# Kernel optimization log

Hardware: AMD Instinct MI355X
Metric: run time of the kernel (lower is better)

## Reference

```python
import jax, jax.numpy as jnp
import numpy as np

V, D, F, K, L, R, ID, B = 50000, 64, 100, 3, 256, 10, 32, 128
IDMAX = 50


def _cnn(vec, Wc, bc, Wl, bl):
    # vec: [N, L, D] -> Conv1d over L (channels=D), ReLU, max-pool over L, Linear+tanh
    x = vec.transpose(0, 2, 1)  # [N, D, L]
    pad = (K - 1) // 2
    y = jax.lax.conv_general_dilated(x, Wc, (1,), [(pad, pad)],
                                     dimension_numbers=('NCH', 'OIH', 'NCH'))
    y = jax.nn.relu(y + bc[None, :, None])  # [N, F, L]
    y = y.max(axis=2)  # [N, F]
    return jnp.tanh(y @ Wl.T + bl)  # [N, ID]


def _fm(x, v, w, b):
    lin = x @ w.T + b  # [N, 1]
    i1 = x @ v
    i2 = (x ** 2) @ (v ** 2)
    pair = jnp.sum(i1 ** 2 - i2, axis=1)
    return (lin[:, 0] + 0.5 * pair)[:, None]


def setup_inputs() -> dict:
    key = jax.random.key(0)
    ks = iter(jax.random.split(key, 40))
    nrm = lambda shape, s=0.1: jax.random.normal(next(ks), shape, jnp.float32) * s
    ri = lambda shape, hi: jax.random.randint(next(ks), shape, 0, hi, dtype=jnp.int32)
    return dict(
        user_reviews=ri((B, R, L), V), item_reviews=ri((B, R, L), V),
        uids=ri((B,), IDMAX), iids=ri((B,), IDMAX),
        user2item=ri((B, R), IDMAX), item2user=ri((B, R), IDMAX),
        rand_reviews=ri((B, L), V),
        user_emb=nrm((V, D)), item_emb=nrm((V, D)),
        cu_Wc=nrm((F, D, K)), cu_bc=jnp.zeros((F,)), cu_Wl=nrm((ID, F)), cu_bl=jnp.zeros((ID,)),
        ci_Wc=nrm((F, D, K)), ci_bc=jnp.zeros((F,)), ci_Wl=nrm((ID, F)), ci_bl=jnp.zeros((ID,)),
        t_W1=nrm((ID, 2 * R * ID)), t_b1=jnp.full((ID,), 0.1),
        t_W2=nrm((ID, ID)), t_b2=jnp.full((ID,), 0.1),
        fs_v=jnp.full((ID, 8), 0.001), fs_w=nrm((1, ID), 0.001), fs_b=jnp.zeros((1,)),
        te_emb=nrm((V, D)),
        tc_Wc=nrm((F, D, K)), tc_bc=jnp.zeros((F,)), tc_Wl=nrm((ID, F)), tc_bl=jnp.zeros((ID,)),
        ft_v=jnp.full((ID, 8), 0.001), ft_w=nrm((1, ID), 0.001), ft_b=jnp.zeros((1,)),
    )


def reference(user_reviews, item_reviews, uids, iids, user2item, item2user, rand_reviews,
              user_emb, item_emb, cu_Wc, cu_bc, cu_Wl, cu_bl, ci_Wc, ci_bc, ci_Wl, ci_bl,
              t_W1, t_b1, t_W2, t_b2, fs_v, fs_w, fs_b,
              te_emb, tc_Wc, tc_bc, tc_Wl, tc_bl, ft_v, ft_w, ft_b):
    Bn = user_reviews.shape[0]
    ur = user_reviews.reshape(Bn * R, L)
    ir = item_reviews.reshape(Bn * R, L)
    # SourceNet
    ul = _cnn(user_emb[ur], cu_Wc, cu_bc, cu_Wl, cu_bl).reshape(Bn, R * ID)
    il = _cnn(item_emb[ir], ci_Wc, ci_bc, ci_Wl, ci_bl).reshape(Bn, R * ID)
    cat = jnp.concatenate([ul, il], axis=1)  # [B, 2*R*ID]
    h = jnp.tanh(cat @ t_W1.T + t_b1)
    src = jnp.tanh(h @ t_W2.T + t_b2)  # dropout in eval mode = identity
    _src_pred = _fm(jax.lax.stop_gradient(src), fs_v, fs_w, fs_b)  # computed, unused in output
    # Vectorized replacement of the per-sample membership/gather loop
    mu = user2item == iids[:, None]  # [B, R]
    mi = item2user == uids[:, None]  # [B, R]
    gu = user_reviews[jnp.arange(Bn), jnp.argmax(mu, axis=1)]  # first match
    gi = item_reviews[jnp.arange(Bn), jnp.argmax(mi, axis=1)]
    reviews = jnp.where(mu.any(1)[:, None], gu,
                        jnp.where(mi.any(1)[:, None], gi, rand_reviews))  # [B, L]
    # TargetNet
    tl = _cnn(te_emb[reviews], tc_Wc, tc_bc, tc_Wl, tc_bl)
    _tgt_pred = _fm(tl, ft_v, ft_w, ft_b)  # computed, unused in output
    return src, tl
```

## Files before the change

kernel.cpp:

```cpp
#include <hip/hip_runtime.h>
#include <hip/hip_bf16.h>


#define C_V 50000
#define C_D 64
#define C_F 100
#define C_K 3
#define C_L 256
#define C_R 10
#define C_ID 32
#define C_B 128

typedef unsigned int u32;
typedef unsigned short u16;
typedef __attribute__((ext_vector_type(8))) short bf16x8;
typedef __attribute__((ext_vector_type(4))) float f32x4;

__device__ __forceinline__ float bf2f(u16 h) { union {u32 u; float f;} v; v.u = ((u32)h) << 16; return v.f; }
__device__ __forceinline__ u16 f2bf(float f) {
    union {float f; u32 u;} v; v.f = f;
    u32 u = v.u;
    return (u16)((u + 0x7fffu + ((u >> 16) & 1u)) >> 16);
}
__device__ __forceinline__ float ldf(const void* p, int idx, int isf) {
    return isf ? ((const float*)p)[idx] : bf2f(((const u16*)p)[idx]);
}
__device__ __forceinline__ void stf(void* p, int idx, float v, int isf) {
    if (isf) ((float*)p)[idx] = v; else ((u16*)p)[idx] = f2bf(v);
}
__device__ __forceinline__ int detect_isf(const u32* __restrict__ ue, int lane) {
    u32 w = ue[lane];
    u32 e = (w >> 7) & 0xFFu;
    int hit = (e >= 0x70u && e <= 0x7Fu);
    unsigned long long m = __ballot(hit);
    return (__popcll(m) >= 32) ? 0 : 1;
}
__device__ __forceinline__ void gl_lds16(const void* g, void* l) {
    __builtin_amdgcn_global_load_lds(
        (const __attribute__((address_space(1))) void*)g,
        (__attribute__((address_space(3))) void*)l, 16, 0, 0);
}

__global__ __launch_bounds__(256) void prep_bfrags(
    const void* __restrict__ cu_Wc, const void* __restrict__ ci_Wc,
    const void* __restrict__ tc_Wc, const u32* __restrict__ ue,
    u16* __restrict__ wsB)
{
    int tid = threadIdx.x;
    int isf = detect_isf(ue, tid & 63);
    int id = blockIdx.x * 256 + tid;
    if (id >= 3 * 6 * 7 * 64) return;
    int s    = id / 2688;
    int rem  = id % 2688;
    int c    = rem / 448;
    int rem2 = rem % 448;
    int nt   = rem2 / 64;
    int lane = rem2 % 64;
    int f    = nt * 16 + (lane & 15);
    int quad = lane >> 4;
    const void* W = (s == 0) ? cu_Wc : (s == 1) ? ci_Wc : tc_Wc;
    u16 out[8];
    #pragma unroll
    for (int j = 0; j < 8; ++j) {
        int kdim = c * 32 + quad * 8 + j;
        int tap = kdim >> 6, d = kdim & 63;
        float v = (f < C_F) ? ldf(W, (f * C_D + d) * C_K + tap, isf) : 0.f;
        out[j] = f2bf(v);
    }
    *reinterpret_cast<uint4*>(wsB + id * 8) = *reinterpret_cast<const uint4*>(out);
}

__global__ __launch_bounds__(256, 4) void cnn_mfma(
    const int* __restrict__ user_reviews, const int* __restrict__ item_reviews,
    const int* __restrict__ uids, const int* __restrict__ iids,
    const int* __restrict__ user2item, const int* __restrict__ item2user,
    const int* __restrict__ rand_reviews,
    const void* __restrict__ user_emb, const void* __restrict__ item_emb,
    const void* __restrict__ te_emb,
    const void* __restrict__ cu_bc, const void* __restrict__ cu_Wl, const void* __restrict__ cu_bl,
    const void* __restrict__ ci_bc, const void* __restrict__ ci_Wl, const void* __restrict__ ci_bl,
    const void* __restrict__ tc_bc, const void* __restrict__ tc_Wl, const void* __restrict__ tc_bl,
    const u16* __restrict__ wsB,
    float* __restrict__ ws_cat, void* __restrict__ d_out)
{
    __shared__ __align__(16) char smem[258 * 128 + 1600];
    u16*   embS  = (u16*)smem;
    float* poolS = (float*)(smem + 258 * 128);
    float* partS = (float*)smem;

    const int tid = threadIdx.x;
    const int idx = (blockIdx.x & 7) * 336 + (blockIdx.x >> 3);
    const int lane = tid & 63, wave = tid >> 6;
    const int isf = detect_isf((const u32*)user_emb, lane);

    const int* toks;
    const void* emb;
    int set;
    const void *bc, *Wl, *bl;

    if (idx < C_B * C_R) {
        toks = user_reviews + idx * C_L;
        emb = user_emb; set = 0;
        bc = cu_bc; Wl = cu_Wl; bl = cu_bl;
    } else if (idx < 2 * C_B * C_R) {
        int j = idx - C_B * C_R;
        toks = item_reviews + j * C_L;
        emb = item_emb; set = 1;
        bc = ci_bc; Wl = ci_Wl; bl = ci_bl;
    } else {
        int b = idx - 2 * C_B * C_R;
        const int* t_ = rand_reviews + b * C_L;
        int iid = iids[b];
        int uid = uids[b];
        int fu = -1, fi = -1;
        for (int r = C_R - 1; r >= 0; --r) {
            if (user2item[b * C_R + r] == iid) fu = r;
            if (item2user[b * C_R + r] == uid) fi = r;
        }
        if (fu >= 0)      t_ = user_reviews + (b * C_R + fu) * C_L;
        else if (fi >= 0) t_ = item_reviews + (b * C_R + fi) * C_L;
        toks = t_;
        emb = te_emb; set = 2;
        bc = tc_bc; Wl = tc_Wl; bl = tc_bl;
    }

    if (tid < 32)            ((u32*)embS)[tid] = 0u;
    else if (tid < 64)       ((u32*)embS)[257 * 32 + (tid - 32)] = 0u;

    if (!isf) {
        int tok64 = toks[wave * 64 + lane];
        const u16* ebp = (const u16*)emb;
        #pragma unroll
        for (int i = 0; i < 8; ++i) {
            int sub = lane >> 3;
            int token = __shfl(tok64, i * 8 + sub);
            int row_lds = wave * 64 + i * 8 + sub + 1;
            int schunk = (lane & 7) ^ (row_lds & 7);
            const void* g = ebp + (size_t)token * C_D + schunk * 8;
            u16* ldsbase = embS + (size_t)(wave * 64 + i * 8 + 1) * 64;
            gl_lds16(g, ldsbase);
        }
    } else {
        int token = toks[tid];
        int rw = (tid + 1) & 7;
        u16* dst = embS + (size_t)(tid + 1) * 64;
        const float4* srow = reinterpret_cast<const float4*>(
            (const float*)emb + (size_t)token * C_D);
        #pragma unroll
        for (int c = 0; c < 8; ++c) {
            float4 a = srow[2 * c];
            float4 b = srow[2 * c + 1];
            u16 t[8] = {f2bf(a.x), f2bf(a.y), f2bf(a.z), f2bf(a.w),
                        f2bf(b.x), f2bf(b.y), f2bf(b.z), f2bf(b.w)};
            *reinterpret_cast<uint4*>(dst + (c ^ rw) * 8) =
                *reinterpret_cast<const uint4*>(t);
        }
    }
    __syncthreads();

    const int quad = lane >> 4, mcol = lane & 15;
    const int mbase = wave * 64;
    const u16* BfG = wsB + set * 21504;

    {
        f32x4 acc[4][4];
        #pragma unroll
        for (int mt = 0; mt < 4; ++mt)
            #pragma unroll
            for (int nt = 0; nt < 4; ++nt) acc[mt][nt] = (f32x4){0.f,0.f,0.f,0.f};
        #pragma unroll
        for (int c = 0; c < 6; ++c) {
            const int tap = c >> 1, dh = c & 1;
            const int schunk = (dh * 4 + quad) ^ ((mcol + tap) & 7);
            bf16x8 bfr[4];
            #pragma unroll
            for (int nt = 0; nt < 4; ++nt)
                bfr[nt] = *reinterpret_cast<const bf16x8*>(BfG + ((c * 7 + nt) * 64 + lane) * 8);
            bf16x8 afr[4];
            #pragma unroll
            for (int mt = 0; mt < 4; ++mt) {
                int row = mbase + mt * 16 + mcol + tap;
                afr[mt] = *reinterpret_cast<const bf16x8*>(embS + row * 64 + schunk * 8);
            }
            #pragma unroll
            for (int mt = 0; mt < 4; ++mt)
                #pragma unroll
                for (int nt = 0; nt < 4; ++nt)
                    acc[mt][nt] = __builtin_amdgcn_mfma_f32_16x16x32_bf16(
                        afr[mt], bfr[nt], acc[mt][nt], 0, 0, 0);
        }
        #pragma unroll
        for (int nt = 0; nt < 4; ++nt) {
            float mv = -1e30f;
            #pragma unroll
            for (int mt = 0; mt < 4; ++mt)
                mv = fmaxf(mv, fmaxf(fmaxf(acc[mt][nt].x, acc[mt][nt].y),
                                     fmaxf(acc[mt][nt].z, acc[mt][nt].w)));
            mv = fmaxf(mv, __shfl_xor(mv, 16));
            mv = fmaxf(mv, __shfl_xor(mv, 32));
            if (quad == 0) poolS[(nt * 16 + mcol) * 4 + wave] = mv;
        }
    }
    {
        f32x4 acc[4][3];
        #pragma unroll
        for (int mt = 0; mt < 4; ++mt)
            #pragma unroll
            for (int nt = 0; nt < 3; ++nt) acc[mt][nt] = (f32x4){0.f,0.f,0.f,0.f};
        #pragma unroll
        for (int c = 0; c < 6; ++c) {
            const int tap = c >> 1, dh = c & 1;
            const int schunk = (dh * 4 + quad) ^ ((mcol + tap) & 7);
            bf16x8 bfr[3];
            #pragma unroll
            for (int nt = 0; nt < 3; ++nt)
                bfr[nt] = *reinterpret_cast<const bf16x8*>(BfG + ((c * 7 + 4 + nt) * 64 + lane) * 8);
            bf16x8 afr[4];
            #pragma unroll
            for (int mt = 0; mt < 4; ++mt) {
                int row = mbase + mt * 16 + mcol + tap;
                afr[mt] = *reinterpret_cast<const bf16x8*>(embS + row * 64 + schunk * 8);
            }
            #pragma unroll
            for (int mt = 0; mt < 4; ++mt)
                #pragma unroll
                for (int nt = 0; nt < 3; ++nt)
                    acc[mt][nt] = __builtin_amdgcn_mfma_f32_16x16x32_bf16(
                        afr[mt], bfr[nt], acc[mt][nt], 0, 0, 0);
        }
        #pragma unroll
        for (int nt = 0; nt < 3; ++nt) {
            float mv = -1e30f;
            #pragma unroll
            for (int mt = 0; mt < 4; ++mt)
                mv = fmaxf(mv, fmaxf(fmaxf(acc[mt][nt].x, acc[mt][nt].y),
                                     fmaxf(acc[mt][nt].z, acc[mt][nt].w)));
            mv = fmaxf(mv, __shfl_xor(mv, 16));
            mv = fmaxf(mv, __shfl_xor(mv, 32));
            int f = (4 + nt) * 16 + mcol;
            if (quad == 0 && f < C_F) poolS[f * 4 + wave] = mv;
        }
    }
    __syncthreads();

    if (tid < C_F) {
        float m4 = fmaxf(fmaxf(poolS[tid * 4 + 0], poolS[tid * 4 + 1]),
                         fmaxf(poolS[tid * 4 + 2], poolS[tid * 4 + 3]));
        poolS[tid * 4] = fmaxf(m4 + ldf(bc, tid, isf), 0.f);
    }
    __syncthreads();

    {
        int o = tid >> 3, seg = tid & 7;
        int f0 = (seg < 4) ? seg * 13 : 52 + (seg - 4) * 12;
        int cnt = (seg < 4) ? 13 : 12;
        float acc = 0.f;
        for (int q = 0; q < cnt; ++q) {
            int f = f0 + q;
            acc += poolS[f * 4] * ldf(Wl, o * C_F + f, isf);
        }
        partS[o * 8 + seg] = acc;
    }
    __syncthreads();
    if (tid < C_ID) {
        float s = ldf(bl, tid, isf);
        #pragma unroll
        for (int q = 0; q < 8; ++q) s += partS[tid * 8 + q];
        float v = tanhf(s);
        if (idx < C_B * C_R) {
            int b = idx / C_R, r = idx % C_R;
            ws_cat[b * 640 + r * C_ID + tid] = v;
        } else if (idx < 2 * C_B * C_R) {
            int j = idx - C_B * C_R;
            int b = j / C_R, r = j % C_R;
            ws_cat[b * 640 + 320 + r * C_ID + tid] = v;
        } else {
            int b = idx - 2 * C_B * C_R;
            stf(d_out, C_B * C_ID + b * C_ID + tid, v, isf);
        }
    }
}

__global__ __launch_bounds__(256) void head_kernel(
    const float* __restrict__ ws_cat,
    const void* __restrict__ W1, const void* __restrict__ b1,
    const void* __restrict__ W2, const void* __restrict__ b2,
    const u32* __restrict__ ue, void* __restrict__ d_out)
{
    __shared__ float part[C_ID][8];
    __shared__ float h_s[C_ID];
    int b = blockIdx.x;
    int tid = threadIdx.x;
    int isf = detect_isf(ue, tid & 63);
    int o = tid >> 3, seg = tid & 7;
    const float* cat = ws_cat + b * 640;
    float acc = 0.f;
    int j0 = seg * 80;
    for (int j = j0; j < j0 + 80; ++j) acc += cat[j] * ldf(W1, o * 640 + j, isf);
    part[o][seg] = acc;
    __syncthreads();
    if (tid < C_ID) {
        float s = ldf(b1, tid, isf);
        #pragma unroll
        for (int q = 0; q < 8; ++q) s += part[tid][q];
        h_s[tid] = tanhf(s);
    }
    __syncthreads();
    if (tid < C_ID) {
        float s = ldf(b2, tid, isf);
        #pragma unroll
        for (int i = 0; i < C_ID; ++i) s += h_s[i] * ldf(W2, tid * C_ID + i, isf);
        stf(d_out, b * C_ID + tid, tanhf(s), isf);
    }
}

extern "C" void kernel_launch(void* const* d_in, const int* in_sizes, int n_in,
                              void* d_out, int out_size, void* d_ws, size_t ws_size,
                              hipStream_t stream)
{
    const int* user_reviews = (const int*)d_in[0];
    const int* item_reviews = (const int*)d_in[1];
    const int* uids         = (const int*)d_in[2];
    const int* iids         = (const int*)d_in[3];
    const int* user2item    = (const int*)d_in[4];
    const int* item2user    = (const int*)d_in[5];
    const int* rand_reviews = (const int*)d_in[6];
    const void* user_emb = d_in[7];
    const void* item_emb = d_in[8];
    const void* cu_Wc = d_in[9];
    const void* cu_bc = d_in[10];
    const void* cu_Wl = d_in[11];
    const void* cu_bl = d_in[12];
    const void* ci_Wc = d_in[13];
    const void* ci_bc = d_in[14];
    const void* ci_Wl = d_in[15];
    const void* ci_bl = d_in[16];
    const void* t_W1  = d_in[17];
    const void* t_b1  = d_in[18];
    const void* t_W2  = d_in[19];
    const void* t_b2  = d_in[20];
    const void* te_emb = d_in[24];
    const void* tc_Wc  = d_in[25];
    const void* tc_bc  = d_in[26];
    const void* tc_Wl  = d_in[27];
    const void* tc_bl  = d_in[28];

    u16*   ws_B   = (u16*)d_ws;
    float* ws_cat = (float*)((char*)d_ws + 129536);

    prep_bfrags<<<32, 256, 0, stream>>>(cu_Wc, ci_Wc, tc_Wc,
                                        (const u32*)user_emb, ws_B);

    cnn_mfma<<<2 * C_B * C_R + C_B, 256, 0, stream>>>(
        user_reviews, item_reviews, uids, iids, user2item, item2user, rand_reviews,
        user_emb, item_emb, te_emb,
        cu_bc, cu_Wl, cu_bl, ci_bc, ci_Wl, ci_bl, tc_bc, tc_Wl, tc_bl,
        ws_B, ws_cat, d_out);

    head_kernel<<<C_B, 256, 0, stream>>>(ws_cat, t_W1, t_b1, t_W2, t_b2,
                                         (const u32*)user_emb, d_out);
}
```

Measured before the change: 205.1 us.

## Give each wave a private halo embedding buffer and overlap gathers with MFMA

Each wave now gathers its own 64 rows plus two halo rows into a private LDS buffer, reading padding rows from a zeroed workspace, so the block-wide barrier after the gather is removed in the bf16 path. The conv GEMM is split into two row halves, and partial vmcnt waits let the first half run while the second half's async loads are still in flight. The final linear reduction now uses wave shuffles instead of an LDS round trip and an extra barrier. This adds LDS per block (the halo rows are duplicated) and relies on hand-written waitcnt ordering being correct.

Result: slower. 307.9 us (+50.1%).

```diff
diff --git a/kernel.cpp b/kernel.cpp
--- a/kernel.cpp
+++ b/kernel.cpp
@@ -44,9 +44,10 @@
 __global__ __launch_bounds__(256) void prep_bfrags(
     const void* __restrict__ cu_Wc, const void* __restrict__ ci_Wc,
     const void* __restrict__ tc_Wc, const u32* __restrict__ ue,
-    u16* __restrict__ wsB)
+    u16* __restrict__ wsB, u32* __restrict__ wsZ)
 {
     int tid = threadIdx.x;
+    if (blockIdx.x == 0 && tid < 32) wsZ[tid] = 0u;
     int isf = detect_isf(ue, tid & 63);
     int id = blockIdx.x * 256 + tid;
     if (id >= 3 * 6 * 7 * 64) return;
@@ -70,6 +71,49 @@
     *reinterpret_cast<uint4*>(wsB + id * 8) = *reinterpret_cast<const uint4*>(out);
 }
 
+template<int NTN>
+__device__ __forceinline__ void gemm_chunk(
+    const u16* __restrict__ waveBuf, const u16* __restrict__ BfG,
+    int mt0, int nt0, int lane, int quad, int mcol, float* perm)
+{
+    f32x4 acc[2][NTN];
+    #pragma unroll
+    for (int m = 0; m < 2; ++m)
+        #pragma unroll
+        for (int n = 0; n < NTN; ++n) acc[m][n] = (f32x4){0.f, 0.f, 0.f, 0.f};
+    #pragma unroll
+    for (int c = 0; c < 6; ++c) {
+        const int tap = c >> 1, dh = c & 1;
+        bf16x8 bfr[NTN];
+        #pragma unroll
+        for (int n = 0; n < NTN; ++n)
+            bfr[n] = *reinterpret_cast<const bf16x8*>(
+                BfG + (size_t)((c * 7 + nt0 + n) * 64 + lane) * 8);
+        bf16x8 afr[2];
+        #pragma unroll
+        for (int m = 0; m < 2; ++m) {
+            int q = (mt0 + m) * 16 + mcol + tap;
+            int slot = (dh * 4 + quad) ^ (q & 7);
+            afr[m] = *reinterpret_cast<const bf16x8*>(waveBuf + q * 64 + slot * 8);
+        }
+        #pragma unroll
+        for (int m = 0; m < 2; ++m)
+            #pragma unroll
+            for (int n = 0; n < NTN; ++n)
+                acc[m][n] = __builtin_amdgcn_mfma_f32_16x16x32_bf16(
+                    afr[m], bfr[n], acc[m][n], 0, 0, 0);
+    }
+    #pragma unroll
+    for (int n = 0; n < NTN; ++n) {
+        float mv = perm[nt0 + n];
+        #pragma unroll
+        for (int m = 0; m < 2; ++m)
+            mv = fmaxf(mv, fmaxf(fmaxf(acc[m][n].x, acc[m][n].y),
+                                 fmaxf(acc[m][n].z, acc[m][n].w)));
+        perm[nt0 + n] = mv;
+    }
+}
+
 __global__ __launch_bounds__(256, 4) void cnn_mfma(
     const int* __restrict__ user_reviews, const int* __restrict__ item_reviews,
     const int* __restrict__ uids, const int* __restrict__ iids,
@@ -80,13 +124,12 @@
     const void* __restrict__ cu_bc, const void* __restrict__ cu_Wl, const void* __restrict__ cu_bl,
     const void* __restrict__ ci_bc, const void* __restrict__ ci_Wl, const void* __restrict__ ci_bl,
     const void* __restrict__ tc_bc, const void* __restrict__ tc_Wl, const void* __restrict__ tc_bl,
-    const u16* __restrict__ wsB,
+    const u16* __restrict__ wsB, const void* __restrict__ wsZ,
     float* __restrict__ ws_cat, void* __restrict__ d_out)
 {
-    __shared__ __align__(16) char smem[258 * 128 + 1600];
+    __shared__ __align__(16) char smem[4 * 72 * 128 + 1600];
     u16*   embS  = (u16*)smem;
-    float* poolS = (float*)(smem + 258 * 128);
-    float* partS = (float*)smem;
+    float* poolS = (float*)(smem + 4 * 72 * 128);
 
     const int tid = threadIdx.x;
     const int idx = (blockIdx.x & 7) * 336 + (blockIdx.x >> 3);
@@ -124,122 +167,85 @@
         bc = tc_bc; Wl = tc_Wl; bl = tc_bl;
     }
 
-    if (tid < 32)            ((u32*)embS)[tid] = 0u;
-    else if (tid < 64)       ((u32*)embS)[257 * 32 + (tid - 32)] = 0u;
+    const int wavebase = wave * 64;
+    u16* waveBuf = embS + (size_t)wave * 72 * 64;
 
     if (!isf) {
-        int tok64 = toks[wave * 64 + lane];
+        int pA = wavebase - 1 + lane;
+        int tokA = toks[pA < 0 ? 0 : pA];
+        int pB = wavebase + 63 + lane;
+        int tokB = toks[pB > 255 ? 255 : pB];
         const u16* ebp = (const u16*)emb;
-        #pragma unroll
-        for (int i = 0; i < 8; ++i) {
+        const u16* zp  = (const u16*)wsZ;
+        #pragma unroll
+        for (int i = 0; i < 9; ++i) {
             int sub = lane >> 3;
-            int token = __shfl(tok64, i * 8 + sub);
-            int row_lds = wave * 64 + i * 8 + sub + 1;
-            int schunk = (lane & 7) ^ (row_lds & 7);
-            const void* g = ebp + (size_t)token * C_D + schunk * 8;
-            u16* ldsbase = embS + (size_t)(wave * 64 + i * 8 + 1) * 64;
-            gl_lds16(g, ldsbase);
+            int q = i * 8 + sub;
+            int schunk = (lane & 7) ^ (sub & 7);
+            int p = wavebase + q - 1;
+            int token = (i < 8) ? __shfl(tokA, q) : __shfl(tokB, q - 64);
+            const u16* g = (p < 0 || p > 255) ? zp + schunk * 8
+                           : ebp + (size_t)token * C_D + schunk * 8;
+            gl_lds16(g, waveBuf + (size_t)i * 8 * 64);
         }
     } else {
-        int token = toks[tid];
-        int rw = (tid + 1) & 7;
-        u16* dst = embS + (size_t)(tid + 1) * 64;
-        const float4* srow = reinterpret_cast<const float4*>(
-            (const float*)emb + (size_t)token * C_D);
-        #pragma unroll
-        for (int c = 0; c < 8; ++c) {
-            float4 a = srow[2 * c];
-            float4 b = srow[2 * c + 1];
-            u16 t[8] = {f2bf(a.x), f2bf(a.y), f2bf(a.z), f2bf(a.w),
-                        f2bf(b.x), f2bf(b.y), f2bf(b.z), f2bf(b.w)};
-            *reinterpret_cast<uint4*>(dst + (c ^ rw) * 8) =
-                *reinterpret_cast<const uint4*>(t);
-        }
-    }
-    __syncthreads();
+        #pragma unroll
+        for (int rep = 0; rep < 2; ++rep) {
+            int q = rep ? 64 + lane : lane;
+            bool act = rep ? (lane < 2) : true;
+            if (act) {
+                int p = wavebase + q - 1;
+                u16* dst = waveBuf + (size_t)q * 64;
+                if (p >= 0 && p <= 255) {
+                    int token = toks[p];
+                    const float4* srow = reinterpret_cast<const float4*>(
+                        (const float*)emb + (size_t)token * C_D);
+                    #pragma unroll
+                    for (int c2 = 0; c2 < 8; ++c2) {
+                        float4 a = srow[2 * c2];
+                        float4 b = srow[2 * c2 + 1];
+                        u16 t[8] = {f2bf(a.x), f2bf(a.y), f2bf(a.z), f2bf(a.w),
+                                    f2bf(b.x), f2bf(b.y), f2bf(b.z), f2bf(b.w)};
+                        *reinterpret_cast<uint4*>(dst + (c2 ^ (q & 7)) * 8) =
+                            *reinterpret_cast<const uint4*>(t);
+                    }
+                } else {
+                    #pragma unroll
+                    for (int c2 = 0; c2 < 8; ++c2)
+                        *reinterpret_cast<uint4*>(dst + c2 * 8) = (uint4){0, 0, 0, 0};
+                }
+            }
+        }
+        __syncthreads();
+    }
 
     const int quad = lane >> 4, mcol = lane & 15;
-    const int mbase = wave * 64;
     const u16* BfG = wsB + set * 21504;
 
-    {
-        f32x4 acc[4][4];
-        #pragma unroll
-        for (int mt = 0; mt < 4; ++mt)
-            #pragma unroll
-            for (int nt = 0; nt < 4; ++nt) acc[mt][nt] = (f32x4){0.f,0.f,0.f,0.f};
-        #pragma unroll
-        for (int c = 0; c < 6; ++c) {
-            const int tap = c >> 1, dh = c & 1;
-            const int schunk = (dh * 4 + quad) ^ ((mcol + tap) & 7);
-            bf16x8 bfr[4];
-            #pragma unroll
-            for (int nt = 0; nt < 4; ++nt)
-                bfr[nt] = *reinterpret_cast<const bf16x8*>(BfG + ((c * 7 + nt) * 64 + lane) * 8);
-            bf16x8 afr[4];
-            #pragma unroll
-            for (int mt = 0; mt < 4; ++mt) {
-                int row = mbase + mt * 16 + mcol + tap;
-                afr[mt] = *reinterpret_cast<const bf16x8*>(embS + row * 64 + schunk * 8);
-            }
-            #pragma unroll
-            for (int mt = 0; mt < 4; ++mt)
-                #pragma unroll
-                for (int nt = 0; nt < 4; ++nt)
-                    acc[mt][nt] = __builtin_amdgcn_mfma_f32_16x16x32_bf16(
-                        afr[mt], bfr[nt], acc[mt][nt], 0, 0, 0);
-        }
-        #pragma unroll
-        for (int nt = 0; nt < 4; ++nt) {
-            float mv = -1e30f;
-            #pragma unroll
-            for (int mt = 0; mt < 4; ++mt)
-                mv = fmaxf(mv, fmaxf(fmaxf(acc[mt][nt].x, acc[mt][nt].y),
-                                     fmaxf(acc[mt][nt].z, acc[mt][nt].w)));
-            mv = fmaxf(mv, __shfl_xor(mv, 16));
-            mv = fmaxf(mv, __shfl_xor(mv, 32));
-            if (quad == 0) poolS[(nt * 16 + mcol) * 4 + wave] = mv;
-        }
-    }
-    {
-        f32x4 acc[4][3];
-        #pragma unroll
-        for (int mt = 0; mt < 4; ++mt)
-            #pragma unroll
-            for (int nt = 0; nt < 3; ++nt) acc[mt][nt] = (f32x4){0.f,0.f,0.f,0.f};
-        #pragma unroll
-        for (int c = 0; c < 6; ++c) {
-            const int tap = c >> 1, dh = c & 1;
-            const int schunk = (dh * 4 + quad) ^ ((mcol + tap) & 7);
-            bf16x8 bfr[3];
-            #pragma unroll
-            for (int nt = 0; nt < 3; ++nt)
-                bfr[nt] = *reinterpret_cast<const bf16x8*>(BfG + ((c * 7 + 4 + nt) * 64 + lane) * 8);
-            bf16x8 afr[4];
-            #pragma unroll
-            for (int mt = 0; mt < 4; ++mt) {
-                int row = mbase + mt * 16 + mcol + tap;
-                afr[mt] = *reinterpret_cast<const bf16x8*>(embS + row * 64 + schunk * 8);
-            }
-            #pragma unroll
-            for (int mt = 0; mt < 4; ++mt)
-                #pragma unroll
-                for (int nt = 0; nt < 3; ++nt)
-                    acc[mt][nt] = __builtin_amdgcn_mfma_f32_16x16x32_bf16(
-                        afr[mt], bfr[nt], acc[mt][nt], 0, 0, 0);
-        }
-        #pragma unroll
-        for (int nt = 0; nt < 3; ++nt) {
-            float mv = -1e30f;
-            #pragma unroll
-            for (int mt = 0; mt < 4; ++mt)
-                mv = fmaxf(mv, fmaxf(fmaxf(acc[mt][nt].x, acc[mt][nt].y),
-                                     fmaxf(acc[mt][nt].z, acc[mt][nt].w)));
-            mv = fmaxf(mv, __shfl_xor(mv, 16));
-            mv = fmaxf(mv, __shfl_xor(mv, 32));
-            int f = (4 + nt) * 16 + mcol;
-            if (quad == 0 && f < C_F) poolS[f * 4 + wave] = mv;
-        }
+    float perm[7];
+    #pragma unroll
+    for (int n = 0; n < 7; ++n) perm[n] = -1e30f;
+
+    if (!isf) {
+        asm volatile("s_waitcnt vmcnt(4)" ::: "memory");
+        __builtin_amdgcn_sched_barrier(0);
+    }
+    gemm_chunk<4>(waveBuf, BfG, 0, 0, lane, quad, mcol, perm);
+    gemm_chunk<3>(waveBuf, BfG, 0, 4, lane, quad, mcol, perm);
+    if (!isf) {
+        asm volatile("s_waitcnt vmcnt(0)" ::: "memory");
+        __builtin_amdgcn_sched_barrier(0);
+    }
+    gemm_chunk<4>(waveBuf, BfG, 2, 0, lane, quad, mcol, perm);
+    gemm_chunk<3>(waveBuf, BfG, 2, 4, lane, quad, mcol, perm);
+
+    #pragma unroll
+    for (int nt = 0; nt < 7; ++nt) {
+        float mv = perm[nt];
+        mv = fmaxf(mv, __shfl_xor(mv, 16));
+        mv = fmaxf(mv, __shfl_xor(mv, 32));
+        int f = nt * 16 + mcol;
+        if (quad == 0 && f < C_F) poolS[f * 4 + wave] = mv;
     }
     __syncthreads();
 
@@ -259,24 +265,22 @@
             int f = f0 + q;
             acc += poolS[f * 4] * ldf(Wl, o * C_F + f, isf);
         }
-        partS[o * 8 + seg] = acc;
-    }
-    __syncthreads();
-    if (tid < C_ID) {
-        float s = ldf(bl, tid, isf);
-        #pragma unroll
-        for (int q = 0; q < 8; ++q) s += partS[tid * 8 + q];
-        float v = tanhf(s);
-        if (idx < C_B * C_R) {
-            int b = idx / C_R, r = idx % C_R;
-            ws_cat[b * 640 + r * C_ID + tid] = v;
-        } else if (idx < 2 * C_B * C_R) {
-            int j = idx - C_B * C_R;
-            int b = j / C_R, r = j % C_R;
-            ws_cat[b * 640 + 320 + r * C_ID + tid] = v;
-        } else {
-            int b = idx - 2 * C_B * C_R;
-            stf(d_out, C_B * C_ID + b * C_ID + tid, v, isf);
+        acc += __shfl_xor(acc, 1);
+        acc += __shfl_xor(acc, 2);
+        acc += __shfl_xor(acc, 4);
+        if (seg == 0) {
+            float v = tanhf(acc + ldf(bl, o, isf));
+            if (idx < C_B * C_R) {
+                int b = idx / C_R, r = idx % C_R;
+                ws_cat[b * 640 + r * C_ID + o] = v;
+            } else if (idx < 2 * C_B * C_R) {
+                int j = idx - C_B * C_R;
+                int b = j / C_R, r = j % C_R;
+                ws_cat[b * 640 + 320 + r * C_ID + o] = v;
+            } else {
+                int b = idx - 2 * C_B * C_R;
+                stf(d_out, C_B * C_ID + b * C_ID + o, v, isf);
+            }
         }
     }
 }
@@ -346,16 +350,17 @@
     const void* tc_bl  = d_in[28];
 
     u16*   ws_B   = (u16*)d_ws;
+    u32*   ws_zero = (u32*)((char*)d_ws + 129024);
     float* ws_cat = (float*)((char*)d_ws + 129536);
 
     prep_bfrags<<<32, 256, 0, stream>>>(cu_Wc, ci_Wc, tc_Wc,
-                                        (const u32*)user_emb, ws_B);
+                                        (const u32*)user_emb, ws_B, ws_zero);
 
     cnn_mfma<<<2 * C_B * C_R + C_B, 256, 0, stream>>>(
         user_reviews, item_reviews, uids, iids, user2item, item2user, rand_reviews,
         user_emb, item_emb, te_emb,
         cu_bc, cu_Wl, cu_bl, ci_bc, ci_Wl, ci_bl, tc_bc, tc_Wl, tc_bl,
-        ws_B, ws_cat, d_out);
+        ws_B, ws_zero, ws_cat, d_out);
 
     head_kernel<<<C_B, 256, 0, stream>>>(ws_cat, t_W1, t_b1, t_W2, t_b2,
                                          (const u32*)user_emb, d_out);
```
